# Kernel tuning notes

Hardware: AMD Instinct MI355X
Metric: run time of the kernel (lower is better)

Reference implementation:

```python
import jax, jax.numpy as jnp
import numpy as np

N = 200_000
MUL = 128          # multiplicity of each irrep block in input
# input layout per e3nn: [128x0e | 128x1o | 128x2e] -> [128 | 384 | 640] = 1152
OFF_1O = MUL       # start of the 1o block
DIM_1O = MUL * 3


def setup_inputs() -> dict:
    key = jax.random.key(0)
    k1, k2, k3 = jax.random.split(key, 3)
    x = jax.random.normal(k1, (N, MUL + MUL * 3 + MUL * 5), dtype=jnp.float32)
    w_lin = jax.random.normal(k2, (MUL, 2), dtype=jnp.float32)  # 128x1o -> 2x1o path
    w_tp = jax.random.normal(k3, (1,), dtype=jnp.float32)       # uvw weight, 1x1x1
    return {"x": x, "w_lin": w_lin, "w_tp": w_tp}


def reference(x, w_lin, w_tp):
    n = x.shape[0]
    # --- o3.Linear(128x0e+128x1o+128x2e -> 2x1o) ---
    # only the 1o block has a path; e3nn 'element' normalization: 1/sqrt(fan_in=128)
    x1o = x[:, OFF_1O:OFF_1O + DIM_1O].reshape(n, MUL, 3)          # [N, 128, 3]
    inv_sqrt_fan = 1.0 / jnp.sqrt(jnp.asarray(MUL, x.dtype))
    y = jnp.einsum('nui,uw->nwi', x1o, w_lin) * inv_sqrt_fan       # [N, 2, 3]
    # --- split into two 1x1o halves (y flattened layout is (mul, dim)) ---
    a = y[:, 0, :]   # [N, 3]
    b = y[:, 1, :]   # [N, 3]
    # --- FullyConnectedTensorProduct(1x1o, 1x1o -> 1x0e) ---
    # wigner_3j(1,1,0)[i,j] = delta_ij / sqrt(3); path_weight = 1
    inv_sqrt3 = 1.0 / jnp.sqrt(jnp.asarray(3.0, x.dtype))
    dot = jnp.sum(a * b, axis=-1, keepdims=True)                   # [N, 1]
    return w_tp[0] * inv_sqrt3 * dot                               # [N, 1]
```

## Files before the change

kernel.cpp:

```cpp
#include <hip/hip_runtime.h>


#define ROW_STRIDE 1152
#define OFF 128

__global__ __launch_bounds__(256) void lintp_kernel(
    const float* __restrict__ x,
    const float* __restrict__ w_lin,
    const float* __restrict__ w_tp,
    float* __restrict__ out,
    int n)
{
    __shared__ float4 tile[16 * 96];

    const int tid = threadIdx.x;
    const int t   = tid & 15;
    const int g   = tid >> 4;
    const int row = blockIdx.x * 16 + g;

    float w0[8], w1[8];
    const float4* wv = (const float4*)(w_lin + 16 * t);
#pragma unroll
    for (int k = 0; k < 4; ++k) {
        float4 w = wv[k];
        w0[2 * k]     = w.x;  w1[2 * k]     = w.y;
        w0[2 * k + 1] = w.z;  w1[2 * k + 1] = w.w;
    }

    const int rowc = (row < n) ? row : (n - 1);
    const float4* xp = (const float4*)(x + (size_t)rowc * ROW_STRIDE + OFF);
    float4 v[6];
#pragma unroll
    for (int k = 0; k < 6; ++k) v[k] = xp[t + 16 * k];
#pragma unroll
    for (int k = 0; k < 6; ++k) tile[g * 96 + t + 16 * k] = v[k];

    __syncthreads();

    float a0 = 0.f, a1 = 0.f, a2 = 0.f, b0 = 0.f, b1 = 0.f, b2 = 0.f;
#pragma unroll
    for (int k = 0; k < 6; ++k) {
        float4 c = tile[g * 96 + 6 * t + k];
        float cc[4] = {c.x, c.y, c.z, c.w};
#pragma unroll
        for (int j = 0; j < 4; ++j) {
            const int p  = 4 * k + j;
            const int i  = p % 3;
            const int ur = p / 3;
            const float av = cc[j];
            if (i == 0)      { a0 += av * w0[ur]; b0 += av * w1[ur]; }
            else if (i == 1) { a1 += av * w0[ur]; b1 += av * w1[ur]; }
            else             { a2 += av * w0[ur]; b2 += av * w1[ur]; }
        }
    }

#pragma unroll
    for (int m = 1; m <= 8; m <<= 1) {
        a0 += __shfl_xor(a0, m); a1 += __shfl_xor(a1, m); a2 += __shfl_xor(a2, m);
        b0 += __shfl_xor(b0, m); b1 += __shfl_xor(b1, m); b2 += __shfl_xor(b2, m);
    }

    if (t == 0 && row < n) {
        const float scale = w_tp[0] / (128.0f * 1.7320508075688772f);
        out[row] = scale * (a0 * b0 + a1 * b1 + a2 * b2);
    }
}

extern "C" void kernel_launch(void* const* d_in, const int* in_sizes, int n_in,
                              void* d_out, int out_size, void* d_ws, size_t ws_size,
                              hipStream_t stream) {
    const float* x     = (const float*)d_in[0];
    const float* w_lin = (const float*)d_in[1];
    const float* w_tp  = (const float*)d_in[2];
    float* out = (float*)d_out;

    const int n = in_sizes[0] / ROW_STRIDE;
    const int blocks = (n + 15) / 16;
    lintp_kernel<<<blocks, 256, 0, stream>>>(x, w_lin, w_tp, out, n);
}
```

Measured before the change: 1.021 ms.

## Replace LDS transpose with direct float2 loads in grid-stride loop

Drops the shared-memory staging tile and barrier, so each thread now reads its own contiguous 12 float2 values (24 floats, i.e. 8 u-indices by 3 components) straight from global memory. The kernel also becomes a grid-stride loop with the grid capped at 2048 blocks, and the scale is computed once per thread. Together these remove LDS traffic and per-block overhead, but each lane now reads 96 contiguous bytes with a 96-byte stride across lanes instead of fully coalesced float4 reads, which may hurt load efficiency.

```diff
diff --git a/kernel.cpp b/kernel.cpp
--- a/kernel.cpp
+++ b/kernel.cpp
@@ -11,12 +11,9 @@
     float* __restrict__ out,
     int n)
 {
-    __shared__ float4 tile[16 * 96];
-
     const int tid = threadIdx.x;
     const int t   = tid & 15;
     const int g   = tid >> 4;
-    const int row = blockIdx.x * 16 + g;
 
     float w0[8], w1[8];
     const float4* wv = (const float4*)(w_lin + 16 * t);
@@ -27,42 +24,49 @@
         w0[2 * k + 1] = w.z;  w1[2 * k + 1] = w.w;
     }
 
-    const int rowc = (row < n) ? row : (n - 1);
-    const float4* xp = (const float4*)(x + (size_t)rowc * ROW_STRIDE + OFF);
-    float4 v[6];
+    const float scale = w_tp[0] * (1.0f / (128.0f * 1.7320508075688772f));
+
+    const int group   = blockIdx.x * 16 + g;
+    const int ngroups = gridDim.x * 16;
+
+    for (int row = group; row < n; row += ngroups) {
+        const float2* xp = (const float2*)(x + (size_t)row * ROW_STRIDE + OFF) + 12 * t;
+        float2 d[12];
 #pragma unroll
-    for (int k = 0; k < 6; ++k) v[k] = xp[t + 16 * k];
+        for (int m = 0; m < 12; ++m) d[m] = xp[m];
+
+        float a0 = 0.f, a1 = 0.f, a2 = 0.f, b0 = 0.f, b1 = 0.f, b2 = 0.f;
 #pragma unroll
-    for (int k = 0; k < 6; ++k) tile[g * 96 + t + 16 * k] = v[k];
-
-    __syncthreads();
-
-    float a0 = 0.f, a1 = 0.f, a2 = 0.f, b0 = 0.f, b1 = 0.f, b2 = 0.f;
-#pragma unroll
-    for (int k = 0; k < 6; ++k) {
-        float4 c = tile[g * 96 + 6 * t + k];
-        float cc[4] = {c.x, c.y, c.z, c.w};
-#pragma unroll
-        for (int j = 0; j < 4; ++j) {
-            const int p  = 4 * k + j;
-            const int i  = p % 3;
-            const int ur = p / 3;
-            const float av = cc[j];
-            if (i == 0)      { a0 += av * w0[ur]; b0 += av * w1[ur]; }
-            else if (i == 1) { a1 += av * w0[ur]; b1 += av * w1[ur]; }
-            else             { a2 += av * w0[ur]; b2 += av * w1[ur]; }
+        for (int m = 0; m < 12; ++m) {
+            const float vx = d[m].x;
+            const float vy = d[m].y;
+            {
+                const int q = 2 * m;
+                const int i = q % 3;
+                const int u = q / 3;
+                if (i == 0)      { a0 += vx * w0[u]; b0 += vx * w1[u]; }
+                else if (i == 1) { a1 += vx * w0[u]; b1 += vx * w1[u]; }
+                else             { a2 += vx * w0[u]; b2 += vx * w1[u]; }
+            }
+            {
+                const int q = 2 * m + 1;
+                const int i = q % 3;
+                const int u = q / 3;
+                if (i == 0)      { a0 += vy * w0[u]; b0 += vy * w1[u]; }
+                else if (i == 1) { a1 += vy * w0[u]; b1 += vy * w1[u]; }
+                else             { a2 += vy * w0[u]; b2 += vy * w1[u]; }
+            }
         }
-    }
 
 #pragma unroll
-    for (int m = 1; m <= 8; m <<= 1) {
-        a0 += __shfl_xor(a0, m); a1 += __shfl_xor(a1, m); a2 += __shfl_xor(a2, m);
-        b0 += __shfl_xor(b0, m); b1 += __shfl_xor(b1, m); b2 += __shfl_xor(b2, m);
-    }
+        for (int m = 1; m <= 8; m <<= 1) {
+            a0 += __shfl_xor(a0, m); a1 += __shfl_xor(a1, m); a2 += __shfl_xor(a2, m);
+            b0 += __shfl_xor(b0, m); b1 += __shfl_xor(b1, m); b2 += __shfl_xor(b2, m);
+        }
 
-    if (t == 0 && row < n) {
-        const float scale = w_tp[0] / (128.0f * 1.7320508075688772f);
-        out[row] = scale * (a0 * b0 + a1 * b1 + a2 * b2);
+        if (t == 0) {
+            out[row] = scale * (a0 * b0 + a1 * b1 + a2 * b2);
+        }
     }
 }
 
@@ -75,6 +79,7 @@
     float* out = (float*)d_out;
 
     const int n = in_sizes[0] / ROW_STRIDE;
-    const int blocks = (n + 15) / 16;
+    int blocks = (n + 15) / 16;
+    if (blocks > 2048) blocks = 2048;
     lintp_kernel<<<blocks, 256, 0, stream>>>(x, w_lin, w_tp, out, n);
 }
```

Measured after the change: 1.102 ms. +8.0%, slower.
